# Kernel optimization log

Measured on AMD Instinct MI355X. Metric: run time of the kernel, lower is better.

Reference implementation:

```python
import jax, jax.numpy as jnp
import numpy as np

N_NODES = 50000
N_EDGES = 800000


def gat_layer(x, src, dst, W, al, ar, b, activation):
    # x: [N, F_in], W: [F_in, H*D], al/ar: [H, D], b: [H*D]
    H, D = al.shape
    n = x.shape[0]
    h = (x @ W).reshape(n, H, D)                      # [N, H, D]
    el = jnp.sum(h * al, axis=-1)                     # [N, H]
    er = jnp.sum(h * ar, axis=-1)                     # [N, H]
    e = jax.nn.leaky_relu(el[src] + er[dst], 0.2)     # [E, H]
    # segment softmax over incoming edges of each dst node
    m = jax.ops.segment_max(e, dst, num_segments=n)   # [N, H]
    ex = jnp.exp(e - m[dst])                          # [E, H]
    s = jax.ops.segment_sum(ex, dst, num_segments=n)  # [N, H]
    a = ex / s[dst]                                   # [E, H]
    msg = h[src] * a[:, :, None]                      # [E, H, D]
    out = jax.ops.segment_sum(msg, dst, num_segments=n) + b.reshape(1, H, D)
    return activation(out) if activation is not None else out


def setup_inputs() -> dict:
    key = jax.random.key(0)
    ks = jax.random.split(key, 12)
    feat = jax.random.normal(ks[0], (N_NODES, 128), dtype=jnp.float32)
    src = jax.random.randint(ks[1], (N_EDGES,), 0, N_NODES)
    dst = jax.random.randint(ks[2], (N_EDGES,), 0, N_NODES)
    sc = 0.1
    return {
        "feat": feat, "src": src, "dst": dst,
        "W1": jax.random.normal(ks[3], (128, 256), jnp.float32) * sc,
        "al1": jax.random.normal(ks[4], (4, 64), jnp.float32) * sc,
        "ar1": jax.random.normal(ks[5], (4, 64), jnp.float32) * sc,
        "b1": jnp.zeros((256,), jnp.float32),
        "W2": jax.random.normal(ks[6], (256, 256), jnp.float32) * sc,
        "al2": jax.random.normal(ks[7], (4, 64), jnp.float32) * sc,
        "ar2": jax.random.normal(ks[8], (4, 64), jnp.float32) * sc,
        "b2": jnp.zeros((256,), jnp.float32),
        "W3": jax.random.normal(ks[9], (256, 8), jnp.float32) * sc,
        "al3": jax.random.normal(ks[10], (1, 8), jnp.float32) * sc,
        "ar3": jax.random.normal(ks[11], (1, 8), jnp.float32) * sc,
        "b3": jnp.zeros((8,), jnp.float32),
    }


def reference(feat, src, dst, W1, al1, ar1, b1, W2, al2, ar2, b2, W3, al3, ar3, b3):
    n = feat.shape[0]
    elu = jax.nn.elu
    h = gat_layer(feat, src, dst, W1, al1, ar1, b1, elu).reshape(n, -1)  # flatten heads
    h = gat_layer(h, src, dst, W2, al2, ar2, b2, elu).reshape(n, -1)
    h = gat_layer(h, src, dst, W3, al3, ar3, b3, None)                   # [N, 1, out]
    return h.mean(axis=1)                                               # head mean -> [N, out]
```

## Files before the change

kernel.cpp:

```cpp
#include <hip/hip_runtime.h>
#include <math.h>


typedef _Float16 half8 __attribute__((ext_vector_type(8)));
typedef _Float16 half4 __attribute__((ext_vector_type(4)));
typedef float    floatx4 __attribute__((ext_vector_type(4)));

#define SLOT_CAP 48

__device__ __forceinline__ float leaky02(float x) { return x > 0.f ? x : 0.2f * x; }

__global__ void build_prep(const int* __restrict__ src, const int* __restrict__ dst,
                           int* __restrict__ cnt, unsigned short* __restrict__ slots,
                           const float* __restrict__ W1, _Float16* __restrict__ W1T,
                           const float* __restrict__ W2, _Float16* __restrict__ W2T,
                           const float* __restrict__ al1, const float* __restrict__ ar1,
                           const float* __restrict__ al2, const float* __restrict__ ar2,
                           _Float16* __restrict__ WlrT1, _Float16* __restrict__ WlrT2,
                           const float* __restrict__ W3, const float* __restrict__ al3,
                           const float* __restrict__ ar3, _Float16* __restrict__ B3T,
                           int E, int GE, int GT) {
    int b = blockIdx.x;
    if (b < GE) {
        int i = b * 256 + threadIdx.x;
        if (i < E) {
            int d = dst[i];
            int p = atomicAdd(&cnt[d], 1);
            if (p < SLOT_CAP) slots[d * SLOT_CAP + p] = (unsigned short)src[i];
        }
    } else if (b < GE + GT) {
        int i = (b - GE) * 256 + threadIdx.x;
        if (i < 128 * 256) {
            int m = i >> 7, k = i & 127;
            W1T[i] = (_Float16)W1[k * 256 + m];
        } else {
            int j = i - 128 * 256;
            if (j < 256 * 256) {
                int m = j >> 8, k = j & 255;
                W2T[j] = (_Float16)W2[k * 256 + m];
            }
        }
    } else {
        int t = (b - GE - GT) * 256 + threadIdx.x;
        if (t < 16 * 128) {
            int k = t & 127, c = t >> 7;
            float v = 0.f;
            if (c < 8) {
                int h = c & 3;
                const float* a = (c < 4 ? al1 : ar1) + h * 64;
                const float* wrow = W1 + k * 256 + h * 64;
                #pragma unroll 8
                for (int d = 0; d < 64; ++d) v += wrow[d] * a[d];
            }
            WlrT1[c * 128 + k] = (_Float16)v;
        } else if (t < 16 * 128 + 16 * 256) {
            int e = t - 16 * 128;
            int k = e & 255, c = e >> 8;
            float v = 0.f;
            if (c < 8) {
                int h = c & 3;
                const float* a = (c < 4 ? al2 : ar2) + h * 64;
                const float* wrow = W2 + k * 256 + h * 64;
                #pragma unroll 8
                for (int d = 0; d < 64; ++d) v += wrow[d] * a[d];
            }
            WlrT2[c * 256 + k] = (_Float16)v;
        } else {
            int f = t - 16 * 128 - 16 * 256;
            if (f < 16 * 256) {
                int k = f & 255, c = f >> 8;
                float v = 0.f;
                if (c < 8) {
                    v = W3[k * 8 + c];
                } else if (c == 8) {
                    #pragma unroll
                    for (int d = 0; d < 8; ++d) v += W3[k * 8 + d] * al3[d];
                } else if (c == 9) {
                    #pragma unroll
                    for (int d = 0; d < 8; ++d) v += W3[k * 8 + d] * ar3[d];
                }
                B3T[c * 256 + k] = (_Float16)v;
            }
        }
    }
}

#define GBM 128
#define GBK 32

template <bool AF32>
__global__ __launch_bounds__(256)
void gemm_mfma(const void* __restrict__ Ap, const _Float16* __restrict__ BT,
               _Float16* __restrict__ C, const _Float16* __restrict__ WlrT,
               float* __restrict__ el, float* __restrict__ er, int N, int K) {
    __shared__ _Float16 As[GBM][GBK + 8];
    __shared__ _Float16 Bs[GBM][GBK + 8];
    int tid  = threadIdx.x;
    int wave = tid >> 6, lane = tid & 63;
    int quad = lane >> 4, l16 = lane & 15;
    int row0 = blockIdx.y * GBM;
    int col0 = blockIdx.x * GBM;
    const bool doLR = (blockIdx.x == 0);

    floatx4 acc[8][2];
    #pragma unroll
    for (int i = 0; i < 8; ++i)
        #pragma unroll
        for (int j = 0; j < 2; ++j)
            #pragma unroll
            for (int e = 0; e < 4; ++e) acc[i][j][e] = 0.f;
    floatx4 accLR[2];
    #pragma unroll
    for (int i = 0; i < 2; ++i)
        #pragma unroll
        for (int e = 0; e < 4; ++e) accLR[i][e] = 0.f;

    for (int k0 = 0; k0 < K; k0 += GBK) {
        if (AF32) {
            const float* Af = (const float*)Ap;
            #pragma unroll
            for (int it = 0; it < 4; ++it) {
                int s = it * 256 + tid;
                int r = s >> 3, off = (s & 7) * 4;
                float4 v = make_float4(0.f, 0.f, 0.f, 0.f);
                int gr = row0 + r;
                if (gr < N) v = *(const float4*)&Af[(size_t)gr * K + k0 + off];
                half4 hv;
                hv[0] = (_Float16)v.x; hv[1] = (_Float16)v.y;
                hv[2] = (_Float16)v.z; hv[3] = (_Float16)v.w;
                *(half4*)&As[r][off] = hv;
            }
        } else {
            const _Float16* Ah = (const _Float16*)Ap;
            #pragma unroll
            for (int it = 0; it < 2; ++it) {
                int s = it * 256 + tid;
                int r = s >> 2, off = (s & 3) * 8;
                half8 v;
                #pragma unroll
                for (int q = 0; q < 8; ++q) v[q] = (_Float16)0.f;
                int gr = row0 + r;
                if (gr < N) v = *(const half8*)&Ah[(size_t)gr * K + k0 + off];
                *(half8*)&As[r][off] = v;
            }
        }
        #pragma unroll
        for (int it = 0; it < 2; ++it) {
            int s = it * 256 + tid;
            int r = s >> 2, off = (s & 3) * 8;
            half8 w = *(const half8*)&BT[(size_t)(col0 + r) * K + k0 + off];
            *(half8*)&Bs[r][off] = w;
        }
        __syncthreads();
        half8 bfrag[2];
        #pragma unroll
        for (int ct = 0; ct < 2; ++ct)
            bfrag[ct] = *(const half8*)&Bs[wave * 32 + ct * 16 + l16][quad * 8];
        half8 lrfrag;
        if (doLR)
            lrfrag = *(const half8*)&WlrT[(size_t)l16 * K + k0 + quad * 8];
        #pragma unroll
        for (int rt = 0; rt < 8; ++rt) {
            half8 afrag = *(const half8*)&As[rt * 16 + l16][quad * 8];
            acc[rt][0] = __builtin_amdgcn_mfma_f32_16x16x32_f16(afrag, bfrag[0], acc[rt][0], 0, 0, 0);
            acc[rt][1] = __builtin_amdgcn_mfma_f32_16x16x32_f16(afrag, bfrag[1], acc[rt][1], 0, 0, 0);
            if (doLR && (rt >> 1) == wave)
                accLR[rt & 1] = __builtin_amdgcn_mfma_f32_16x16x32_f16(afrag, lrfrag, accLR[rt & 1], 0, 0, 0);
        }
        __syncthreads();
    }
    #pragma unroll
    for (int rt = 0; rt < 8; ++rt) {
        #pragma unroll
        for (int reg = 0; reg < 4; ++reg) {
            int gr = row0 + rt * 16 + quad * 4 + reg;
            if (gr < N) {
                #pragma unroll
                for (int ct = 0; ct < 2; ++ct) {
                    int gc = col0 + wave * 32 + ct * 16 + l16;
                    C[(size_t)gr * 256 + gc] = (_Float16)acc[rt][ct][reg];
                }
            }
        }
    }
    if (doLR) {
        #pragma unroll
        for (int i = 0; i < 2; ++i) {
            int rt = wave * 2 + i;
            #pragma unroll
            for (int reg = 0; reg < 4; ++reg) {
                int gr = row0 + rt * 16 + quad * 4 + reg;
                if (gr < N) {
                    float v = accLR[i][reg];
                    if (l16 < 4)      el[gr * 4 + l16] = v;
                    else if (l16 < 8) er[gr * 4 + (l16 - 4)] = v;
                }
            }
        }
    }
}

__global__ __launch_bounds__(256)
void gemm3_mfma(const _Float16* __restrict__ x, const _Float16* __restrict__ B3T,
                float* __restrict__ h3, float* __restrict__ el3,
                float* __restrict__ er3, int N) {
    int tid = threadIdx.x;
    int wave = tid >> 6, lane = tid & 63;
    int quad = lane >> 4, l16 = lane & 15;
    int row0 = blockIdx.x * 64 + wave * 16;
    floatx4 acc;
    #pragma unroll
    for (int e = 0; e < 4; ++e) acc[e] = 0.f;
    const _Float16* Ab = x + (size_t)(row0 + l16) * 256 + quad * 8;
    const _Float16* Bb = B3T + (size_t)l16 * 256 + quad * 8;
    #pragma unroll
    for (int ks = 0; ks < 8; ++ks) {
        half8 a = *(const half8*)(Ab + ks * 32);
        half8 bf = *(const half8*)(Bb + ks * 32);
        acc = __builtin_amdgcn_mfma_f32_16x16x32_f16(a, bf, acc, 0, 0, 0);
    }
    #pragma unroll
    for (int reg = 0; reg < 4; ++reg) {
        int r = row0 + quad * 4 + reg;
        if (r < N) {
            float v = acc[reg];
            if (l16 < 8)       h3[(size_t)r * 8 + l16] = v;
            else if (l16 == 8) el3[r] = v;
            else if (l16 == 9) er3[r] = v;
        }
    }
}

__global__ __launch_bounds__(256)
void gat_agg(const _Float16* __restrict__ h16, const float* __restrict__ el,
             const float* __restrict__ er, const int* __restrict__ cnt,
             const unsigned short* __restrict__ slots, const float* __restrict__ bias,
             _Float16* __restrict__ out, int N) {
    __shared__ int   sbuf[8][32];
    __shared__ float wbuf[8][32][4];
    int tid = threadIdx.x;
    int l32 = tid & 31;
    int g = tid >> 5;
    int node = blockIdx.x * 8 + g;
    if (node >= N) return;
    int beg = node * SLOT_CAP;

    int sv = (int)slots[beg + l32];
    float4 ern4 = *(const float4*)&er[node * 4];
    int deg = min(cnt[node], SLOT_CAP);
    float4 elv = *(const float4*)&el[sv * 4];
    int end = beg + deg;
    int hd = l32 >> 3;

    float er0 = ern4.x, er1 = ern4.y, er2 = ern4.z, er3 = ern4.w;
    const _Float16* hb = h16 + l32 * 8;
    float acc[8] = {};

    if (deg <= 32) {
        bool act = l32 < deg;
        float e0 = act ? leaky02(elv.x + er0) : -INFINITY;
        float e1 = act ? leaky02(elv.y + er1) : -INFINITY;
        float e2 = act ? leaky02(elv.z + er2) : -INFINITY;
        float e3 = act ? leaky02(elv.w + er3) : -INFINITY;
        float m0 = e0, m1 = e1, m2 = e2, m3 = e3;
        #pragma unroll
        for (int msk = 1; msk < 32; msk <<= 1) {
            m0 = fmaxf(m0, __shfl_xor(m0, msk));
            m1 = fmaxf(m1, __shfl_xor(m1, msk));
            m2 = fmaxf(m2, __shfl_xor(m2, msk));
            m3 = fmaxf(m3, __shfl_xor(m3, msk));
        }
        float x0 = act ? __expf(e0 - m0) : 0.f;
        float x1 = act ? __expf(e1 - m1) : 0.f;
        float x2 = act ? __expf(e2 - m2) : 0.f;
        float x3 = act ? __expf(e3 - m3) : 0.f;
        float s0 = x0, s1 = x1, s2 = x2, s3 = x3;
        #pragma unroll
        for (int msk = 1; msk < 32; msk <<= 1) {
            s0 += __shfl_xor(s0, msk);
            s1 += __shfl_xor(s1, msk);
            s2 += __shfl_xor(s2, msk);
            s3 += __shfl_xor(s3, msk);
        }
        float i0 = s0 > 0.f ? 1.f / s0 : 0.f;
        float i1 = s1 > 0.f ? 1.f / s1 : 0.f;
        float i2 = s2 > 0.f ? 1.f / s2 : 0.f;
        float i3 = s3 > 0.f ? 1.f / s3 : 0.f;
        if (act) {
            sbuf[g][l32] = sv;
            wbuf[g][l32][0] = x0 * i0;
            wbuf[g][l32][1] = x1 * i1;
            wbuf[g][l32][2] = x2 * i2;
            wbuf[g][l32][3] = x3 * i3;
        }
        int t = 0;
        for (; t + 8 <= deg; t += 8) {
            int sA = sbuf[g][t],     sB = sbuf[g][t + 1];
            int sC = sbuf[g][t + 2], sD = sbuf[g][t + 3];
            int sE = sbuf[g][t + 4], sF = sbuf[g][t + 5];
            int sG = sbuf[g][t + 6], sH = sbuf[g][t + 7];
            float wA = wbuf[g][t][hd],     wB = wbuf[g][t + 1][hd];
            float wC = wbuf[g][t + 2][hd], wD = wbuf[g][t + 3][hd];
            float wE = wbuf[g][t + 4][hd], wF = wbuf[g][t + 5][hd];
            float wG = wbuf[g][t + 6][hd], wH = wbuf[g][t + 7][hd];
            half8 vA = *(const half8*)&hb[(size_t)sA * 256];
            half8 vB = *(const half8*)&hb[(size_t)sB * 256];
            half8 vC = *(const half8*)&hb[(size_t)sC * 256];
            half8 vD = *(const half8*)&hb[(size_t)sD * 256];
            half8 vE = *(const half8*)&hb[(size_t)sE * 256];
            half8 vF = *(const half8*)&hb[(size_t)sF * 256];
            half8 vG = *(const half8*)&hb[(size_t)sG * 256];
            half8 vH = *(const half8*)&hb[(size_t)sH * 256];
            #pragma unroll
            for (int q = 0; q < 8; ++q)
                acc[q] += wA * (float)vA[q] + wB * (float)vB[q]
                        + wC * (float)vC[q] + wD * (float)vD[q]
                        + wE * (float)vE[q] + wF * (float)vF[q]
                        + wG * (float)vG[q] + wH * (float)vH[q];
        }
        for (; t + 4 <= deg; t += 4) {
            int sa = sbuf[g][t],     sb = sbuf[g][t + 1];
            int sc = sbuf[g][t + 2], sd = sbuf[g][t + 3];
            float wa = wbuf[g][t][hd],     wb = wbuf[g][t + 1][hd];
            float wc = wbuf[g][t + 2][hd], wd = wbuf[g][t + 3][hd];
            half8 va = *(const half8*)&hb[(size_t)sa * 256];
            half8 vb = *(const half8*)&hb[(size_t)sb * 256];
            half8 vc = *(const half8*)&hb[(size_t)sc * 256];
            half8 vd = *(const half8*)&hb[(size_t)sd * 256];
            #pragma unroll
            for (int q = 0; q < 8; ++q)
                acc[q] += wa * (float)va[q] + wb * (float)vb[q]
                        + wc * (float)vc[q] + wd * (float)vd[q];
        }
        for (; t < deg; ++t) {
            int s = sbuf[g][t];
            float w = wbuf[g][t][hd];
            half8 v = *(const half8*)&hb[(size_t)s * 256];
            #pragma unroll
            for (int q = 0; q < 8; ++q) acc[q] += w * (float)v[q];
        }
    } else {
        float m0 = -INFINITY, m1 = -INFINITY, m2 = -INFINITY, m3 = -INFINITY;
        for (int j = beg + l32; j < end; j += 32) {
            int s = slots[j];
            float4 ev = *(const float4*)&el[s * 4];
            m0 = fmaxf(m0, leaky02(ev.x + er0));
            m1 = fmaxf(m1, leaky02(ev.y + er1));
            m2 = fmaxf(m2, leaky02(ev.z + er2));
            m3 = fmaxf(m3, leaky02(ev.w + er3));
        }
        #pragma unroll
        for (int msk = 1; msk < 32; msk <<= 1) {
            m0 = fmaxf(m0, __shfl_xor(m0, msk));
            m1 = fmaxf(m1, __shfl_xor(m1, msk));
            m2 = fmaxf(m2, __shfl_xor(m2, msk));
            m3 = fmaxf(m3, __shfl_xor(m3, msk));
        }
        float s0 = 0.f, s1 = 0.f, s2 = 0.f, s3 = 0.f;
        for (int j = beg + l32; j < end; j += 32) {
            int s = slots[j];
            float4 ev = *(const float4*)&el[s * 4];
            s0 += __expf(leaky02(ev.x + er0) - m0);
            s1 += __expf(leaky02(ev.y + er1) - m1);
            s2 += __expf(leaky02(ev.z + er2) - m2);
            s3 += __expf(leaky02(ev.w + er3) - m3);
        }
        #pragma unroll
        for (int msk = 1; msk < 32; msk <<= 1) {
            s0 += __shfl_xor(s0, msk);
            s1 += __shfl_xor(s1, msk);
            s2 += __shfl_xor(s2, msk);
            s3 += __shfl_xor(s3, msk);
        }
        float mh  = (hd & 2) ? ((hd & 1) ? m3 : m2) : ((hd & 1) ? m1 : m0);
        float sh_ = (hd & 2) ? ((hd & 1) ? s3 : s2) : ((hd & 1) ? s1 : s0);
        float erh = (hd & 2) ? ((hd & 1) ? er3 : er2) : ((hd & 1) ? er1 : er0);
        float ih  = sh_ > 0.f ? 1.f / sh_ : 0.f;
        int j = beg;
        for (; j + 4 <= end; j += 4) {
            int sa = slots[j], sb = slots[j + 1], sc = slots[j + 2], sd = slots[j + 3];
            float wa = __expf(leaky02(el[sa * 4 + hd] + erh) - mh) * ih;
            float wb = __expf(leaky02(el[sb * 4 + hd] + erh) - mh) * ih;
            float wc = __expf(leaky02(el[sc * 4 + hd] + erh) - mh) * ih;
            float wd = __expf(leaky02(el[sd * 4 + hd] + erh) - mh) * ih;
            half8 va = *(const half8*)&hb[(size_t)sa * 256];
            half8 vb = *(const half8*)&hb[(size_t)sb * 256];
            half8 vc = *(const half8*)&hb[(size_t)sc * 256];
            half8 vd = *(const half8*)&hb[(size_t)sd * 256];
            #pragma unroll
            for (int q = 0; q < 8; ++q)
                acc[q] += wa * (float)va[q] + wb * (float)vb[q]
                        + wc * (float)vc[q] + wd * (float)vd[q];
        }
        for (; j < end; ++j) {
            int s = slots[j];
            float w = __expf(leaky02(el[s * 4 + hd] + erh) - mh) * ih;
            half8 v = *(const half8*)&hb[(size_t)s * 256];
            #pragma unroll
            for (int q = 0; q < 8; ++q) acc[q] += w * (float)v[q];
        }
    }

    half8 o;
    #pragma unroll
    for (int q = 0; q < 8; ++q) {
        float v = acc[q] + bias[l32 * 8 + q];
        v = v > 0.f ? v : (__expf(v) - 1.f);
        o[q] = (_Float16)v;
    }
    *(half8*)&out[(size_t)node * 256 + l32 * 8] = o;
}

__global__ __launch_bounds__(256)
void gat_agg3(const float* __restrict__ h3, const float* __restrict__ el,
              const float* __restrict__ er, const int* __restrict__ cnt,
              const unsigned short* __restrict__ slots, const float* __restrict__ bias,
              float* __restrict__ out, int N) {
    __shared__ int   sbuf3[4][64];
    __shared__ float wbuf3[4][64];
    int tid = threadIdx.x;
    int lane = tid & 63;
    int wv = tid >> 6;
    int n = blockIdx.x * 4 + wv;
    if (n >= N) return;
    int beg = n * SLOT_CAP;
    int sv = (lane < SLOT_CAP) ? (int)slots[beg + lane] : 0;
    int deg = min(cnt[n], SLOT_CAP);
    float er_n = er[n];
    float elv = el[sv];
    int g = lane >> 3, c = lane & 7;
    float acc = 0.f;
    bool act = lane < deg;
    float e = act ? leaky02(elv + er_n) : -INFINITY;
    float mx = e;
    #pragma unroll
    for (int o = 1; o < 64; o <<= 1) mx = fmaxf(mx, __shfl_xor(mx, o));
    float ex = act ? __expf(e - mx) : 0.f;
    float sm = ex;
    #pragma unroll
    for (int o = 1; o < 64; o <<= 1) sm += __shfl_xor(sm, o);
    float inv = sm > 0.f ? 1.f / sm : 0.f;
    if (act) {
        sbuf3[wv][lane] = sv;
        wbuf3[wv][lane] = ex * inv;
    }
    for (int t = g; t < deg; t += 8) {
        int s = sbuf3[wv][t];
        float w = wbuf3[wv][t];
        acc += h3[s * 8 + c] * w;
    }
    acc += __shfl_xor(acc, 8);
    acc += __shfl_xor(acc, 16);
    acc += __shfl_xor(acc, 32);
    if (lane < 8) out[(size_t)n * 8 + lane] = acc + bias[lane];
}

static inline size_t align_up(size_t x, size_t a) { return (x + a - 1) & ~(a - 1); }

extern "C" void kernel_launch(void* const* d_in, const int* in_sizes, int n_in,
                              void* d_out, int out_size, void* d_ws, size_t ws_size,
                              hipStream_t stream) {
    const float* feat = (const float*)d_in[0];
    const int*   src  = (const int*)d_in[1];
    const int*   dst  = (const int*)d_in[2];
    const float* W1   = (const float*)d_in[3];
    const float* al1  = (const float*)d_in[4];
    const float* ar1  = (const float*)d_in[5];
    const float* b1   = (const float*)d_in[6];
    const float* W2   = (const float*)d_in[7];
    const float* al2  = (const float*)d_in[8];
    const float* ar2  = (const float*)d_in[9];
    const float* b2   = (const float*)d_in[10];
    const float* W3   = (const float*)d_in[11];
    const float* al3  = (const float*)d_in[12];
    const float* ar3  = (const float*)d_in[13];
    const float* b3   = (const float*)d_in[14];

    const int N = in_sizes[0] / 128;
    const int E = in_sizes[1];

    char* w = (char*)d_ws;
    _Float16* bufA16 = (_Float16*)w; w += align_up((size_t)N * 256 * 2, 256);
    _Float16* bufB16 = (_Float16*)w; w += align_up((size_t)N * 256 * 2, 256);
    _Float16* W1T    = (_Float16*)w; w += align_up((size_t)256 * 128 * 2, 256);
    _Float16* W2T    = (_Float16*)w; w += align_up((size_t)256 * 256 * 2, 256);
    _Float16* WlrT1  = (_Float16*)w; w += align_up((size_t)16 * 128 * 2, 256);
    _Float16* WlrT2  = (_Float16*)w; w += align_up((size_t)16 * 256 * 2, 256);
    _Float16* B3T    = (_Float16*)w; w += align_up((size_t)16 * 256 * 2, 256);
    float* el      = (float*)w; w += align_up((size_t)N * 4 * 4, 256);
    float* er      = (float*)w; w += align_up((size_t)N * 4 * 4, 256);
    float* el3     = (float*)w; w += align_up((size_t)N * 4, 256);
    float* er3     = (float*)w; w += align_up((size_t)N * 4, 256);
    float* h3      = (float*)w; w += align_up((size_t)N * 8 * 4, 256);
    int*   cnt     = (int*)w;   w += align_up((size_t)N * 4, 256);
    unsigned short* slots = (unsigned short*)w;
    w += align_up((size_t)N * SLOT_CAP * 2, 256);
    (void)ws_size; (void)n_in; (void)out_size;

    const int GE = (E + 255) / 256;
    const int GT = (128 * 256 + 256 * 256 + 255) / 256;
    const int GG = (16 * 128 + 16 * 256 + 16 * 256 + 255) / 256;

    (void)hipMemsetAsync(cnt, 0, (size_t)N * 4, stream);
    build_prep<<<GE + GT + GG, 256, 0, stream>>>(src, dst, cnt, slots,
                                                 W1, W1T, W2, W2T,
                                                 al1, ar1, al2, ar2,
                                                 WlrT1, WlrT2,
                                                 W3, al3, ar3, B3T, E, GE, GT);

    dim3 ggrid(2, (N + GBM - 1) / GBM);
    const int GA = (N + 7) / 8;

    gemm_mfma<true><<<ggrid, 256, 0, stream>>>(feat, W1T, bufA16, WlrT1, el, er, N, 128);
    gat_agg<<<GA, 256, 0, stream>>>(bufA16, el, er, cnt, slots, b1, bufB16, N);

    gemm_mfma<false><<<ggrid, 256, 0, stream>>>(bufB16, W2T, bufA16, WlrT2, el, er, N, 256);
    gat_agg<<<GA, 256, 0, stream>>>(bufA16, el, er, cnt, slots, b2, bufB16, N);

    gemm3_mfma<<<(N + 63) / 64, 256, 0, stream>>>(bufB16, B3T, h3, el3, er3, N);
    gat_agg3<<<(N + 3) / 4, 256, 0, stream>>>(h3, el3, er3, cnt, slots, b3,
                                              (float*)d_out, N);
}
```

Baseline: 349.4 us.

## Split GAT aggregation into per-head channel slices with edge-parallel lanes

Replaces the per-node aggregation kernel, in which 32 lanes each own 8 channels and walk every edge serially, with a sliced kernel. Each block slice now handles 32 channels of one head. Within that slice, 8 clusters of 4 lanes process different edges in parallel and combine results with cross-lane shuffle reductions. The goal is more parallelism and shorter serial gather chains per node. The cost is 8x more blocks, softmax logits recomputed for every slice, and nontemporal loads and stores. The old path for degree above 32 is removed and every node is capped at SLOT_CAP edges.

Measured after the change: 472.3 us. +35.2%, slower.

```diff
diff --git a/kernel.cpp b/kernel.cpp
--- a/kernel.cpp
+++ b/kernel.cpp
@@ -232,183 +232,75 @@
 }
 
 __global__ __launch_bounds__(256)
-void gat_agg(const _Float16* __restrict__ h16, const float* __restrict__ el,
-             const float* __restrict__ er, const int* __restrict__ cnt,
-             const unsigned short* __restrict__ slots, const float* __restrict__ bias,
-             _Float16* __restrict__ out, int N) {
-    __shared__ int   sbuf[8][32];
-    __shared__ float wbuf[8][32][4];
+void gat_agg_slice(const _Float16* __restrict__ h16, const float* __restrict__ el,
+                   const float* __restrict__ er, const int* __restrict__ cnt,
+                   const unsigned short* __restrict__ slots, const float* __restrict__ bias,
+                   _Float16* __restrict__ out, int N) {
+    __shared__ int   ssb[8][SLOT_CAP];
+    __shared__ float wwb[8][SLOT_CAP];
     int tid = threadIdx.x;
     int l32 = tid & 31;
     int g = tid >> 5;
-    int node = blockIdx.x * 8 + g;
+    int slice = blockIdx.x & 7;
+    int node = (blockIdx.x >> 3) * 8 + g;
     if (node >= N) return;
     int beg = node * SLOT_CAP;
-
-    int sv = (int)slots[beg + l32];
-    float4 ern4 = *(const float4*)&er[node * 4];
+    int hd = slice >> 1;
+    int chbase = slice * 32;
+    int cluster = l32 >> 2, pos = l32 & 3;
+
+    int sv0 = (int)__builtin_nontemporal_load(&slots[beg + l32]);
     int deg = min(cnt[node], SLOT_CAP);
-    float4 elv = *(const float4*)&el[sv * 4];
-    int end = beg + deg;
-    int hd = l32 >> 3;
-
-    float er0 = ern4.x, er1 = ern4.y, er2 = ern4.z, er3 = ern4.w;
-    const _Float16* hb = h16 + l32 * 8;
+    float er_h = er[node * 4 + hd];
+    int j1 = 32 + (l32 & 15);
+    int sv1 = (int)__builtin_nontemporal_load(&slots[beg + j1]);
+    float e0v = el[sv0 * 4 + hd];
+    float e1v = el[sv1 * 4 + hd];
+    bool v0 = l32 < deg;
+    bool v1 = (l32 < 16) && (j1 < deg);
+    float e0 = v0 ? leaky02(e0v + er_h) : -INFINITY;
+    float e1 = v1 ? leaky02(e1v + er_h) : -INFINITY;
+    float m = fmaxf(e0, e1);
+    #pragma unroll
+    for (int msk = 1; msk < 32; msk <<= 1) m = fmaxf(m, __shfl_xor(m, msk));
+    float x0 = v0 ? __expf(e0 - m) : 0.f;
+    float x1 = v1 ? __expf(e1 - m) : 0.f;
+    float s = x0 + x1;
+    #pragma unroll
+    for (int msk = 1; msk < 32; msk <<= 1) s += __shfl_xor(s, msk);
+    float inv = s > 0.f ? 1.f / s : 0.f;
+    ssb[g][l32] = sv0;
+    wwb[g][l32] = x0 * inv;
+    if (l32 < 16) { ssb[g][j1] = sv1; wwb[g][j1] = x1 * inv; }
+
     float acc[8] = {};
-
-    if (deg <= 32) {
-        bool act = l32 < deg;
-        float e0 = act ? leaky02(elv.x + er0) : -INFINITY;
-        float e1 = act ? leaky02(elv.y + er1) : -INFINITY;
-        float e2 = act ? leaky02(elv.z + er2) : -INFINITY;
-        float e3 = act ? leaky02(elv.w + er3) : -INFINITY;
-        float m0 = e0, m1 = e1, m2 = e2, m3 = e3;
-        #pragma unroll
-        for (int msk = 1; msk < 32; msk <<= 1) {
-            m0 = fmaxf(m0, __shfl_xor(m0, msk));
-            m1 = fmaxf(m1, __shfl_xor(m1, msk));
-            m2 = fmaxf(m2, __shfl_xor(m2, msk));
-            m3 = fmaxf(m3, __shfl_xor(m3, msk));
-        }
-        float x0 = act ? __expf(e0 - m0) : 0.f;
-        float x1 = act ? __expf(e1 - m1) : 0.f;
-        float x2 = act ? __expf(e2 - m2) : 0.f;
-        float x3 = act ? __expf(e3 - m3) : 0.f;
-        float s0 = x0, s1 = x1, s2 = x2, s3 = x3;
-        #pragma unroll
-        for (int msk = 1; msk < 32; msk <<= 1) {
-            s0 += __shfl_xor(s0, msk);
-            s1 += __shfl_xor(s1, msk);
-            s2 += __shfl_xor(s2, msk);
-            s3 += __shfl_xor(s3, msk);
-        }
-        float i0 = s0 > 0.f ? 1.f / s0 : 0.f;
-        float i1 = s1 > 0.f ? 1.f / s1 : 0.f;
-        float i2 = s2 > 0.f ? 1.f / s2 : 0.f;
-        float i3 = s3 > 0.f ? 1.f / s3 : 0.f;
-        if (act) {
-            sbuf[g][l32] = sv;
-            wbuf[g][l32][0] = x0 * i0;
-            wbuf[g][l32][1] = x1 * i1;
-            wbuf[g][l32][2] = x2 * i2;
-            wbuf[g][l32][3] = x3 * i3;
-        }
-        int t = 0;
-        for (; t + 8 <= deg; t += 8) {
-            int sA = sbuf[g][t],     sB = sbuf[g][t + 1];
-            int sC = sbuf[g][t + 2], sD = sbuf[g][t + 3];
-            int sE = sbuf[g][t + 4], sF = sbuf[g][t + 5];
-            int sG = sbuf[g][t + 6], sH = sbuf[g][t + 7];
-            float wA = wbuf[g][t][hd],     wB = wbuf[g][t + 1][hd];
-            float wC = wbuf[g][t + 2][hd], wD = wbuf[g][t + 3][hd];
-            float wE = wbuf[g][t + 4][hd], wF = wbuf[g][t + 5][hd];
-            float wG = wbuf[g][t + 6][hd], wH = wbuf[g][t + 7][hd];
-            half8 vA = *(const half8*)&hb[(size_t)sA * 256];
-            half8 vB = *(const half8*)&hb[(size_t)sB * 256];
-            half8 vC = *(const half8*)&hb[(size_t)sC * 256];
-            half8 vD = *(const half8*)&hb[(size_t)sD * 256];
-            half8 vE = *(const half8*)&hb[(size_t)sE * 256];
-            half8 vF = *(const half8*)&hb[(size_t)sF * 256];
-            half8 vG = *(const half8*)&hb[(size_t)sG * 256];
-            half8 vH = *(const half8*)&hb[(size_t)sH * 256];
-            #pragma unroll
-            for (int q = 0; q < 8; ++q)
-                acc[q] += wA * (float)vA[q] + wB * (float)vB[q]
-                        + wC * (float)vC[q] + wD * (float)vD[q]
-                        + wE * (float)vE[q] + wF * (float)vF[q]
-                        + wG * (float)vG[q] + wH * (float)vH[q];
-        }
-        for (; t + 4 <= deg; t += 4) {
-            int sa = sbuf[g][t],     sb = sbuf[g][t + 1];
-            int sc = sbuf[g][t + 2], sd = sbuf[g][t + 3];
-            float wa = wbuf[g][t][hd],     wb = wbuf[g][t + 1][hd];
-            float wc = wbuf[g][t + 2][hd], wd = wbuf[g][t + 3][hd];
-            half8 va = *(const half8*)&hb[(size_t)sa * 256];
-            half8 vb = *(const half8*)&hb[(size_t)sb * 256];
-            half8 vc = *(const half8*)&hb[(size_t)sc * 256];
-            half8 vd = *(const half8*)&hb[(size_t)sd * 256];
-            #pragma unroll
-            for (int q = 0; q < 8; ++q)
-                acc[q] += wa * (float)va[q] + wb * (float)vb[q]
-                        + wc * (float)vc[q] + wd * (float)vd[q];
-        }
-        for (; t < deg; ++t) {
-            int s = sbuf[g][t];
-            float w = wbuf[g][t][hd];
-            half8 v = *(const half8*)&hb[(size_t)s * 256];
-            #pragma unroll
-            for (int q = 0; q < 8; ++q) acc[q] += w * (float)v[q];
-        }
-    } else {
-        float m0 = -INFINITY, m1 = -INFINITY, m2 = -INFINITY, m3 = -INFINITY;
-        for (int j = beg + l32; j < end; j += 32) {
-            int s = slots[j];
-            float4 ev = *(const float4*)&el[s * 4];
-            m0 = fmaxf(m0, leaky02(ev.x + er0));
-            m1 = fmaxf(m1, leaky02(ev.y + er1));
-            m2 = fmaxf(m2, leaky02(ev.z + er2));
-            m3 = fmaxf(m3, leaky02(ev.w + er3));
-        }
-        #pragma unroll
-        for (int msk = 1; msk < 32; msk <<= 1) {
-            m0 = fmaxf(m0, __shfl_xor(m0, msk));
-            m1 = fmaxf(m1, __shfl_xor(m1, msk));
-            m2 = fmaxf(m2, __shfl_xor(m2, msk));
-            m3 = fmaxf(m3, __shfl_xor(m3, msk));
-        }
-        float s0 = 0.f, s1 = 0.f, s2 = 0.f, s3 = 0.f;
-        for (int j = beg + l32; j < end; j += 32) {
-            int s = slots[j];
-            float4 ev = *(const float4*)&el[s * 4];
-            s0 += __expf(leaky02(ev.x + er0) - m0);
-            s1 += __expf(leaky02(ev.y + er1) - m1);
-            s2 += __expf(leaky02(ev.z + er2) - m2);
-            s3 += __expf(leaky02(ev.w + er3) - m3);
-        }
-        #pragma unroll
-        for (int msk = 1; msk < 32; msk <<= 1) {
-            s0 += __shfl_xor(s0, msk);
-            s1 += __shfl_xor(s1, msk);
-            s2 += __shfl_xor(s2, msk);
-            s3 += __shfl_xor(s3, msk);
-        }
-        float mh  = (hd & 2) ? ((hd & 1) ? m3 : m2) : ((hd & 1) ? m1 : m0);
-        float sh_ = (hd & 2) ? ((hd & 1) ? s3 : s2) : ((hd & 1) ? s1 : s0);
-        float erh = (hd & 2) ? ((hd & 1) ? er3 : er2) : ((hd & 1) ? er1 : er0);
-        float ih  = sh_ > 0.f ? 1.f / sh_ : 0.f;
-        int j = beg;
-        for (; j + 4 <= end; j += 4) {
-            int sa = slots[j], sb = slots[j + 1], sc = slots[j + 2], sd = slots[j + 3];
-            float wa = __expf(leaky02(el[sa * 4 + hd] + erh) - mh) * ih;
-            float wb = __expf(leaky02(el[sb * 4 + hd] + erh) - mh) * ih;
-            float wc = __expf(leaky02(el[sc * 4 + hd] + erh) - mh) * ih;
-            float wd = __expf(leaky02(el[sd * 4 + hd] + erh) - mh) * ih;
-            half8 va = *(const half8*)&hb[(size_t)sa * 256];
-            half8 vb = *(const half8*)&hb[(size_t)sb * 256];
-            half8 vc = *(const half8*)&hb[(size_t)sc * 256];
-            half8 vd = *(const half8*)&hb[(size_t)sd * 256];
-            #pragma unroll
-            for (int q = 0; q < 8; ++q)
-                acc[q] += wa * (float)va[q] + wb * (float)vb[q]
-                        + wc * (float)vc[q] + wd * (float)vd[q];
-        }
-        for (; j < end; ++j) {
-            int s = slots[j];
-            float w = __expf(leaky02(el[s * 4 + hd] + erh) - mh) * ih;
-            half8 v = *(const half8*)&hb[(size_t)s * 256];
-            #pragma unroll
-            for (int q = 0; q < 8; ++q) acc[q] += w * (float)v[q];
-        }
-    }
-
-    half8 o;
+    const _Float16* hb = h16 + chbase + pos * 8;
+    for (int t = 0; t < deg; t += 8) {
+        int j = t + cluster;
+        bool a = j < deg;
+        int svj = ssb[g][a ? j : 0];
+        float wj = a ? wwb[g][j] : 0.f;
+        half8 v = *(const half8*)&hb[(size_t)svj * 256];
+        #pragma unroll
+        for (int q = 0; q < 8; ++q) acc[q] += wj * (float)v[q];
+    }
+
     #pragma unroll
     for (int q = 0; q < 8; ++q) {
-        float v = acc[q] + bias[l32 * 8 + q];
-        v = v > 0.f ? v : (__expf(v) - 1.f);
-        o[q] = (_Float16)v;
-    }
-    *(half8*)&out[(size_t)node * 256 + l32 * 8] = o;
+        acc[q] += __shfl_xor(acc[q], 4);
+        acc[q] += __shfl_xor(acc[q], 8);
+        acc[q] += __shfl_xor(acc[q], 16);
+    }
+    if (l32 < 4) {
+        half8 o;
+        #pragma unroll
+        for (int q = 0; q < 8; ++q) {
+            float v = acc[q] + bias[chbase + pos * 8 + q];
+            v = v > 0.f ? v : (__expf(v) - 1.f);
+            o[q] = (_Float16)v;
+        }
+        __builtin_nontemporal_store(o, (half8*)&out[(size_t)node * 256 + chbase + pos * 8]);
+    }
 }
 
 __global__ __launch_bounds__(256)
@@ -509,13 +401,13 @@
                                                  W3, al3, ar3, B3T, E, GE, GT);
 
     dim3 ggrid(2, (N + GBM - 1) / GBM);
-    const int GA = (N + 7) / 8;
+    const int GAS = 8 * ((N + 7) / 8);
 
     gemm_mfma<true><<<ggrid, 256, 0, stream>>>(feat, W1T, bufA16, WlrT1, el, er, N, 128);
-    gat_agg<<<GA, 256, 0, stream>>>(bufA16, el, er, cnt, slots, b1, bufB16, N);
+    gat_agg_slice<<<GAS, 256, 0, stream>>>(bufA16, el, er, cnt, slots, b1, bufB16, N);
 
     gemm_mfma<false><<<ggrid, 256, 0, stream>>>(bufB16, W2T, bufA16, WlrT2, el, er, N, 256);
-    gat_agg<<<GA, 256, 0, stream>>>(bufA16, el, er, cnt, slots, b2, bufB16, N);
+    gat_agg_slice<<<GAS, 256, 0, stream>>>(bufA16, el, er, cnt, slots, b2, bufB16, N);
 
     gemm3_mfma<<<(N + 63) / 64, 256, 0, stream>>>(bufB16, B3T, h3, el3, er3, N);
     gat_agg3<<<(N + 3) / 4, 256, 0, stream>>>(h3, el3, er3, cnt, slots, b3,
```
